# Optimization experiments

Measured on AMD Instinct MI355X. Metric: run time of the kernel, lower is better.

## Reference

```python
import jax, jax.numpy as jnp
import numpy as np

CH = 512
HEADS = 8
REDUCTION = 2
INNER = max(CH // REDUCTION, HEADS)  # 256
POS_RES = 16
LN_EPS = 1e-5


def setup_inputs() -> dict:
    key = jax.random.key(0)
    ks = jax.random.split(key, 7)
    B, H, W = 1, 64, 64
    x = jax.random.normal(ks[0], (B, CH, H, W), dtype=jnp.float32)
    w_qkv = jax.random.normal(ks[1], (INNER * 3, CH), dtype=jnp.float32) * 0.02
    w_proj = jax.random.normal(ks[2], (CH, INNER), dtype=jnp.float32) * 0.02
    b_proj = jnp.zeros((CH,), dtype=jnp.float32)
    pos_bias = jax.random.normal(ks[3], (1, HEADS, POS_RES, POS_RES), dtype=jnp.float32) * 0.02
    gamma = jnp.ones((CH,), dtype=jnp.float32)
    beta = jnp.zeros((CH,), dtype=jnp.float32)
    return {"x": x, "w_qkv": w_qkv, "w_proj": w_proj, "b_proj": b_proj,
            "pos_bias": pos_bias, "gamma": gamma, "beta": beta}


def reference(x, w_qkv, w_proj, b_proj, pos_bias, gamma, beta):
    B, C, H, W = x.shape
    d_head = INNER // HEADS
    scale = jnp.float32(d_head ** -0.5)

    # 1x1 conv == channel matmul
    qkv = jnp.einsum('oc,bchw->bohw', w_qkv, x)  # [B, 3*inner, H, W]
    q, k, v = jnp.split(qkv, 3, axis=1)

    def heads_view(t):
        return t.reshape(B, HEADS, d_head, H * W)  # [B, h, d, HW]

    q, k, v = heads_view(q), heads_view(k), heads_view(v)

    attn = jnp.einsum('bhdi,bhdj->bhij', q * scale, k)  # [B, h, HW, HW]

    # bilinear interp of pos bias 16x16 -> HxW (half-pixel, matches align_corners=False)
    pos = jax.image.resize(pos_bias, (1, HEADS, H, W), method='bilinear')
    pos = pos.reshape(1, HEADS, H * W)
    attn = attn + pos[..., :, None] + pos[..., None, :]

    attn = jax.nn.softmax(attn, axis=-1)
    y = jnp.einsum('bhij,bhdj->bhdi', attn, v)  # [B, h, d, HW]
    y = y.reshape(B, INNER, H, W)

    y = jnp.einsum('co,bohw->bchw', w_proj, y) + b_proj[None, :, None, None]

    # LayerNorm over channel dim of (x + y)
    z = (x + y).transpose(0, 2, 3, 1)  # [B, H, W, C]
    mu = jnp.mean(z, axis=-1, keepdims=True)
    var = jnp.var(z, axis=-1, keepdims=True)
    z = (z - mu) / jnp.sqrt(var + LN_EPS) * gamma + beta
    return z.transpose(0, 3, 1, 2)
```

## Files before the change

### kernel.cpp

```cpp
#include <hip/hip_runtime.h>
#include <hip/hip_bf16.h>
#include <math.h>

#define HW 4096
#define LN_EPS 1e-5f

typedef _Float16 half4v __attribute__((ext_vector_type(4)));
typedef _Float16 half8v __attribute__((ext_vector_type(8)));
typedef float float4v __attribute__((ext_vector_type(4)));

#if __has_builtin(__builtin_amdgcn_exp2f)
#define EXP2F(x) __builtin_amdgcn_exp2f(x)
#else
#define EXP2F(x) exp2f(x)
#endif

__device__ __forceinline__ half4v lo4(half8v v) { return __builtin_shufflevector(v, v, 0, 1, 2, 3); }
__device__ __forceinline__ half4v hi4(half8v v) { return __builtin_shufflevector(v, v, 4, 5, 6, 7); }

__global__ void k_prep(const float* __restrict__ wq, const float* __restrict__ wp,
                       const float* __restrict__ pb,
                       _Float16* __restrict__ wqh, _Float16* __restrict__ wph,
                       float* __restrict__ pos) {
    const float qs = 0.17677669529663687f * 1.4426950408889634f;
    int i = blockIdx.x * 256 + threadIdx.x;
    if (i < 49152) {
        float s = (i < 16384) ? qs : 1.0f;
        float4v a = *(const float4v*)(wq + i * 8);
        float4v b = *(const float4v*)(wq + i * 8 + 4);
        half8v h;
        #pragma unroll
        for (int k = 0; k < 4; k++) { h[k] = (_Float16)(a[k] * s); h[4 + k] = (_Float16)(b[k] * s); }
        *(half8v*)(wqh + i * 8) = h;
    } else if (i < 65536) {
        int j = i - 49152;
        float4v a = *(const float4v*)(wp + j * 8);
        float4v b = *(const float4v*)(wp + j * 8 + 4);
        half8v h;
        #pragma unroll
        for (int k = 0; k < 4; k++) { h[k] = (_Float16)a[k]; h[4 + k] = (_Float16)b[k]; }
        *(half8v*)(wph + j * 8) = h;
    } else {
        int j = i - 65536;
        int h = j >> 12, p = j & 4095, y = p >> 6, x = p & 63;
        float sy = y * 0.25f - 0.375f, sx = x * 0.25f - 0.375f;
        float fy = floorf(sy), fx = floorf(sx);
        float wy = sy - fy, wx = sx - fx;
        int y0 = (int)fy, x0 = (int)fx;
        int y1 = y0 + 1 < 15 ? y0 + 1 : 15;
        int x1 = x0 + 1 < 15 ? x0 + 1 : 15;
        y0 = y0 > 0 ? y0 : 0;
        x0 = x0 > 0 ? x0 : 0;
        const float* src = pb + h * 256;
        float v = (1.f - wy) * ((1.f - wx) * src[y0 * 16 + x0] + wx * src[y0 * 16 + x1]) +
                  wy * ((1.f - wx) * src[y1 * 16 + x0] + wx * src[y1 * 16 + x1]);
        pos[j] = v * 1.4426950408889634f;
    }
}

__global__ __launch_bounds__(256) void k_xt(const float* __restrict__ x,
                                            _Float16* __restrict__ xt) {
    __shared__ _Float16 tile[64][65];
    int c0 = (blockIdx.x >> 6) * 64;
    int p0 = (blockIdx.x & 63) * 64;
    int t = threadIdx.x, w = t >> 6, lane = t & 63;
    #pragma unroll
    for (int r = 0; r < 16; r++)
        tile[w * 16 + r][lane] = (_Float16)x[(c0 + w * 16 + r) * HW + p0 + lane];
    __syncthreads();
    #pragma unroll
    for (int r = 0; r < 16; r++)
        xt[(p0 + w * 16 + r) * 512 + c0 + lane] = tile[lane][w * 16 + r];
}

__global__ __launch_bounds__(256) void k_qkv(const _Float16* __restrict__ wqh,
                                             const _Float16* __restrict__ xt,
                                             _Float16* __restrict__ qa,
                                             _Float16* __restrict__ ka,
                                             _Float16* __restrict__ va) {
    int n0 = (blockIdx.x >> 5) * 64;
    int p0 = (blockIdx.x & 31) * 128;
    int t = threadIdx.x, w = t >> 6, lane = t & 63, quad = lane >> 4, l16 = lane & 15;

    const _Float16* aptr0 = xt + (p0 + w * 16 + l16) * 512 + quad * 8;
    const _Float16* aptr1 = aptr0 + 64 * 512;
    const _Float16* bptr = wqh + (n0 + l16) * 512 + quad * 8;

    float4v acc[2][4] = {};
    #pragma unroll 4
    for (int kc = 0; kc < 16; kc++) {
        half8v a0 = *(const half8v*)(aptr0 + kc * 32);
        half8v a1 = *(const half8v*)(aptr1 + kc * 32);
        #pragma unroll
        for (int nt = 0; nt < 4; nt++) {
            half8v b = *(const half8v*)(bptr + nt * 16 * 512 + kc * 32);
            acc[0][nt] = __builtin_amdgcn_mfma_f32_16x16x32_f16(a0, b, acc[0][nt], 0, 0, 0);
            acc[1][nt] = __builtin_amdgcn_mfma_f32_16x16x32_f16(a1, b, acc[1][nt], 0, 0, 0);
        }
    }
    #pragma unroll
    for (int ps = 0; ps < 2; ps++) {
        #pragma unroll
        for (int nt = 0; nt < 4; nt++) {
            int o = n0 + nt * 16 + l16;
            #pragma unroll
            for (int r = 0; r < 4; r++) {
                int p = p0 + ps * 64 + w * 16 + quad * 4 + r;
                _Float16 v = (_Float16)acc[ps][nt][r];
                if (o < 256) {
                    qa[(o >> 5) * 131072 + p * 32 + (o & 31)] = v;
                } else if (o < 512) {
                    int oc = o - 256, hh = oc >> 5, d = oc & 31;
                    ka[hh * 131072 + (p >> 4) * 512 + ((d >> 3) * 16 + (p & 15)) * 8 + (d & 7)] = v;
                } else {
                    int oc = o - 512, hh = oc >> 5, d = oc & 31;
                    va[hh * 131072 + (p >> 4) * 512 + (((p >> 2) & 3) * 16 + (d & 15)) * 8 +
                       (d >> 4) * 4 + (p & 3)] = v;
                }
            }
        }
    }
}

__global__ __launch_bounds__(256) void k_attn(const _Float16* __restrict__ qa,
                                              const _Float16* __restrict__ ka,
                                              const _Float16* __restrict__ va,
                                              const float* __restrict__ pos,
                                              float* __restrict__ op,
                                              float* __restrict__ lp) {
    __shared__ __attribute__((aligned(16))) _Float16 kbuf[2][2048];
    __shared__ __attribute__((aligned(16))) _Float16 vbuf[2][2048];
    __shared__ __attribute__((aligned(16))) float posl[2048];
    int h = blockIdx.x & 7;
    int jh = (blockIdx.x >> 3) & 1;
    int qb = blockIdx.x >> 4;
    int t = threadIdx.x, w = t >> 6, lane = t & 63, quad = lane >> 4, l16 = lane & 15;
    int q0 = qb * 128 + w * 32;

    float* opp = op + jh * 1048576;
    float* lpp = lp + jh * 32768;

    {
        const float* ps_ = pos + h * HW + jh * 2048;
        *(float4v*)(posl + t * 8) = *(const float4v*)(ps_ + t * 8);
        *(float4v*)(posl + t * 8 + 4) = *(const float4v*)(ps_ + t * 8 + 4);
    }
    half8v qf0 = *(const half8v*)(qa + h * 131072 + (q0 + l16) * 32 + quad * 8);
    half8v qf1 = *(const half8v*)(qa + h * 131072 + (q0 + 16 + l16) * 32 + quad * 8);

    const _Float16* kg = ka + h * 131072 + jh * 65536;
    const _Float16* vg = va + h * 131072 + jh * 65536;

    half8v kreg = *(const half8v*)(kg + t * 8);
    half8v vreg = *(const half8v*)(vg + t * 8);

    float4v o00 = {}, o01 = {}, o10 = {}, o11 = {};
    float lsum0 = 0.f, lsum1 = 0.f;
    const float4v zero = {0.f, 0.f, 0.f, 0.f};

    for (int tile = 0; tile < 32; tile++) {
        int buf = tile & 1;
        *(half8v*)(kbuf[buf] + t * 8) = kreg;
        *(half8v*)(vbuf[buf] + t * 8) = vreg;
        __syncthreads();
        if (tile + 1 < 32) {
            kreg = *(const half8v*)(kg + (tile + 1) * 2048 + t * 8);
            vreg = *(const half8v*)(vg + (tile + 1) * 2048 + t * 8);
        }
        #pragma unroll
        for (int w16 = 0; w16 < 4; w16++) {
            half8v kf = *(const half8v*)(kbuf[buf] + w16 * 512 + lane * 8);
            half8v vf = *(const half8v*)(vbuf[buf] + w16 * 512 + lane * 8);
            float4v pb = *(const float4v*)(posl + tile * 64 + w16 * 16 + quad * 4);

            float4v s0 = __builtin_amdgcn_mfma_f32_16x16x32_f16(kf, qf0, zero, 0, 0, 0);
            float4v s1 = __builtin_amdgcn_mfma_f32_16x16x32_f16(kf, qf1, zero, 0, 0, 0);

            float e0 = EXP2F(s0[0] + pb[0]);
            float e1 = EXP2F(s0[1] + pb[1]);
            float e2 = EXP2F(s0[2] + pb[2]);
            float e3 = EXP2F(s0[3] + pb[3]);
            float f0 = EXP2F(s1[0] + pb[0]);
            float f1 = EXP2F(s1[1] + pb[1]);
            float f2 = EXP2F(s1[2] + pb[2]);
            float f3 = EXP2F(s1[3] + pb[3]);
            lsum0 += (e0 + e1) + (e2 + e3);
            lsum1 += (f0 + f1) + (f2 + f3);

            half4v pa0, pa1;
            pa0[0] = (_Float16)e0; pa0[1] = (_Float16)e1;
            pa0[2] = (_Float16)e2; pa0[3] = (_Float16)e3;
            pa1[0] = (_Float16)f0; pa1[1] = (_Float16)f1;
            pa1[2] = (_Float16)f2; pa1[3] = (_Float16)f3;

            o00 = __builtin_amdgcn_mfma_f32_16x16x16f16(pa0, lo4(vf), o00, 0, 0, 0);
            o01 = __builtin_amdgcn_mfma_f32_16x16x16f16(pa0, hi4(vf), o01, 0, 0, 0);
            o10 = __builtin_amdgcn_mfma_f32_16x16x16f16(pa1, lo4(vf), o10, 0, 0, 0);
            o11 = __builtin_amdgcn_mfma_f32_16x16x16f16(pa1, hi4(vf), o11, 0, 0, 0);
        }
    }
    lsum0 += __shfl_xor(lsum0, 16, 64);
    lsum0 += __shfl_xor(lsum0, 32, 64);
    lsum1 += __shfl_xor(lsum1, 16, 64);
    lsum1 += __shfl_xor(lsum1, 32, 64);
    #pragma unroll
    for (int r = 0; r < 4; r++) {
        int qr = quad * 4 + r;
        int qi0 = q0 + qr, qi1 = q0 + 16 + qr;
        opp[qi0 * 256 + h * 32 + l16] = o00[r];
        opp[qi0 * 256 + h * 32 + 16 + l16] = o01[r];
        opp[qi1 * 256 + h * 32 + l16] = o10[r];
        opp[qi1 * 256 + h * 32 + 16 + l16] = o11[r];
    }
    if (quad == 0) {
        lpp[(q0 + l16) * 8 + h] = lsum0;
        lpp[(q0 + 16 + l16) * 8 + h] = lsum1;
    }
}

__global__ __launch_bounds__(1024) void k_proj_ln(const _Float16* __restrict__ wph,
                                                  const float* __restrict__ op,
                                                  const float* __restrict__ lp,
                                                  const float* __restrict__ x,
                                                  const float* __restrict__ b_proj,
                                                  const float* __restrict__ gamma,
                                                  const float* __restrict__ beta,
                                                  float* __restrict__ out) {
    __shared__ __attribute__((aligned(16))) _Float16 ys[16 * 264];
    __shared__ float red[2][16][17];
    int p0 = blockIdx.x * 16;
    int t = threadIdx.x, w = t >> 6, lane = t & 63, quad = lane >> 4, l16 = lane & 15;
    {
        int p = t >> 6;
        int cg = (t & 63) * 4;
        int pi = p0 + p;
        float4v a = *(const float4v*)(op + pi * 256 + cg);
        float4v b = *(const float4v*)(op + 1048576 + pi * 256 + cg);
        int hh = cg >> 5;
        float l = lp[pi * 8 + hh] + lp[32768 + pi * 8 + hh];
        float inv = 1.f / l;
        half4v y;
        #pragma unroll
        for (int k = 0; k < 4; k++) y[k] = (_Float16)((a[k] + b[k]) * inv);
        *(half4v*)(ys + p * 264 + cg) = y;
    }
    __syncthreads();
    float4v acc[2] = {};
    #pragma unroll
    for (int kc = 0; kc < 8; kc++) {
        half8v b = *(const half8v*)(ys + l16 * 264 + kc * 32 + quad * 8);
        #pragma unroll
        for (int mt = 0; mt < 2; mt++) {
            half8v a = *(const half8v*)(wph + (w * 32 + mt * 16 + l16) * 256 + kc * 32 + quad * 8);
            acc[mt] = __builtin_amdgcn_mfma_f32_16x16x32_f16(a, b, acc[mt], 0, 0, 0);
        }
    }
    int p = p0 + l16;
    float sum = 0.f, sumsq = 0.f;
    #pragma unroll
    for (int mt = 0; mt < 2; mt++)
        #pragma unroll
        for (int r = 0; r < 4; r++) {
            int c = w * 32 + mt * 16 + quad * 4 + r;
            float v = acc[mt][r] + b_proj[c] + x[c * HW + p];
            acc[mt][r] = v;
            sum += v;
            sumsq += v * v;
        }
    sum += __shfl_xor(sum, 16, 64);
    sum += __shfl_xor(sum, 32, 64);
    sumsq += __shfl_xor(sumsq, 16, 64);
    sumsq += __shfl_xor(sumsq, 32, 64);
    if (quad == 0) { red[0][w][l16] = sum; red[1][w][l16] = sumsq; }
    __syncthreads();
    float s0 = 0.f, s1 = 0.f;
    #pragma unroll
    for (int ww = 0; ww < 16; ww++) { s0 += red[0][ww][l16]; s1 += red[1][ww][l16]; }
    float mean = s0 * (1.f / 512.f);
    float var = s1 * (1.f / 512.f) - mean * mean;
    float rstd = rsqrtf(var + LN_EPS);
    #pragma unroll
    for (int mt = 0; mt < 2; mt++)
        #pragma unroll
        for (int r = 0; r < 4; r++) {
            int c = w * 32 + mt * 16 + quad * 4 + r;
            out[c * HW + p] = (acc[mt][r] - mean) * rstd * gamma[c] + beta[c];
        }
}

extern "C" void kernel_launch(void* const* d_in, const int* in_sizes, int n_in,
                              void* d_out, int out_size, void* d_ws, size_t ws_size,
                              hipStream_t stream) {
    const float* x      = (const float*)d_in[0];
    const float* w_qkv  = (const float*)d_in[1];
    const float* w_proj = (const float*)d_in[2];
    const float* b_proj = (const float*)d_in[3];
    const float* pos_b  = (const float*)d_in[4];
    const float* gamma  = (const float*)d_in[5];
    const float* beta   = (const float*)d_in[6];
    char* ws = (char*)d_ws;
    _Float16* xt  = (_Float16*)(ws);
    _Float16* qa  = (_Float16*)(ws + 4194304);
    _Float16* ka  = (_Float16*)(ws + 6291456);
    _Float16* va  = (_Float16*)(ws + 8388608);
    float*    op  = (float*)   (ws + 10485760);
    float*    lp  = (float*)   (ws + 18874368);
    float*    pos = (float*)   (ws + 19136512);
    _Float16* wqh = (_Float16*)(ws + 19267584);
    _Float16* wph = (_Float16*)(ws + 20054016);

    k_prep<<<384, 256, 0, stream>>>(w_qkv, w_proj, pos_b, wqh, wph, pos);
    k_xt<<<512, 256, 0, stream>>>(x, xt);
    k_qkv<<<384, 256, 0, stream>>>(wqh, xt, qa, ka, va);
    k_attn<<<512, 256, 0, stream>>>(qa, ka, va, pos, op, lp);
    k_proj_ln<<<256, 1024, 0, stream>>>(wph, op, lp, x, b_proj, gamma, beta, (float*)d_out);
}
```

Measured before the change: 151.0 us.

## Split attention keys four ways, fuse prep kernels, use direct LDS loads

Merges the transpose and weight-prep kernels into one launch and vectorizes the transpose stores. Attention now splits the key range into four chunks instead of two, doubling the grid to 1024 blocks with a 4-blocks-per-CU launch bound. It streams K/V tiles straight into LDS with global_load_lds, folds the position bias into the MFMA accumulator input, and uses packed conversions plus fdot2 for the row sums. The projection kernel then reduces four partial outputs, which costs more workspace and more partial-sum traffic.

```diff
diff --git a/kernel.cpp b/kernel.cpp
--- a/kernel.cpp
+++ b/kernel.cpp
@@ -8,6 +8,8 @@
 typedef _Float16 half4v __attribute__((ext_vector_type(4)));
 typedef _Float16 half8v __attribute__((ext_vector_type(8)));
 typedef float float4v __attribute__((ext_vector_type(4)));
+typedef __fp16 fp16v2 __attribute__((ext_vector_type(2)));
+typedef __fp16 fp16v4 __attribute__((ext_vector_type(4)));
 
 #if __has_builtin(__builtin_amdgcn_exp2f)
 #define EXP2F(x) __builtin_amdgcn_exp2f(x)
@@ -18,12 +20,47 @@
 __device__ __forceinline__ half4v lo4(half8v v) { return __builtin_shufflevector(v, v, 0, 1, 2, 3); }
 __device__ __forceinline__ half4v hi4(half8v v) { return __builtin_shufflevector(v, v, 4, 5, 6, 7); }
 
-__global__ void k_prep(const float* __restrict__ wq, const float* __restrict__ wp,
-                       const float* __restrict__ pb,
-                       _Float16* __restrict__ wqh, _Float16* __restrict__ wph,
-                       float* __restrict__ pos) {
+__device__ __forceinline__ void gload_lds16(const _Float16* g, _Float16* l) {
+#if __has_builtin(__builtin_amdgcn_global_load_lds)
+    __builtin_amdgcn_global_load_lds(
+        (const __attribute__((address_space(1))) void*)(const void*)g,
+        (__attribute__((address_space(3))) void*)(void*)l, 16, 0, 0);
+#else
+    int lane = threadIdx.x & 63;
+    *(half8v*)(l + lane * 8) = *(const half8v*)g;
+#endif
+}
+
+__global__ __launch_bounds__(256) void k_pre(const float* __restrict__ x,
+                                             const float* __restrict__ wq,
+                                             const float* __restrict__ wp,
+                                             const float* __restrict__ pb,
+                                             _Float16* __restrict__ xt,
+                                             _Float16* __restrict__ wqh,
+                                             _Float16* __restrict__ wph,
+                                             float* __restrict__ pos) {
+    int bx = blockIdx.x, t = threadIdx.x;
+    if (bx < 512) {
+        __shared__ _Float16 tile[64][65];
+        int c0 = (bx >> 6) * 64, p0 = (bx & 63) * 64;
+        int w = t >> 6, lane = t & 63;
+        #pragma unroll
+        for (int r = 0; r < 16; r++)
+            tile[w * 16 + r][lane] = (_Float16)x[(c0 + w * 16 + r) * HW + p0 + lane];
+        __syncthreads();
+        int cg = (t & 15) * 4, pr = t >> 4;
+        #pragma unroll
+        for (int r = 0; r < 4; r++) {
+            int p = pr + r * 16;
+            half4v v;
+            #pragma unroll
+            for (int k = 0; k < 4; k++) v[k] = tile[cg + k][p];
+            *(half4v*)&xt[(p0 + p) * 512 + c0 + cg] = v;
+        }
+        return;
+    }
+    int i = (bx - 512) * 256 + t;
     const float qs = 0.17677669529663687f * 1.4426950408889634f;
-    int i = blockIdx.x * 256 + threadIdx.x;
     if (i < 49152) {
         float s = (i < 16384) ? qs : 1.0f;
         float4v a = *(const float4v*)(wq + i * 8);
@@ -42,8 +79,8 @@
         *(half8v*)(wph + j * 8) = h;
     } else {
         int j = i - 65536;
-        int h = j >> 12, p = j & 4095, y = p >> 6, x = p & 63;
-        float sy = y * 0.25f - 0.375f, sx = x * 0.25f - 0.375f;
+        int h = j >> 12, p = j & 4095, y = p >> 6, xx = p & 63;
+        float sy = y * 0.25f - 0.375f, sx = xx * 0.25f - 0.375f;
         float fy = floorf(sy), fx = floorf(sx);
         float wy = sy - fy, wx = sx - fx;
         int y0 = (int)fy, x0 = (int)fx;
@@ -56,21 +93,6 @@
                   wy * ((1.f - wx) * src[y1 * 16 + x0] + wx * src[y1 * 16 + x1]);
         pos[j] = v * 1.4426950408889634f;
     }
-}
-
-__global__ __launch_bounds__(256) void k_xt(const float* __restrict__ x,
-                                            _Float16* __restrict__ xt) {
-    __shared__ _Float16 tile[64][65];
-    int c0 = (blockIdx.x >> 6) * 64;
-    int p0 = (blockIdx.x & 63) * 64;
-    int t = threadIdx.x, w = t >> 6, lane = t & 63;
-    #pragma unroll
-    for (int r = 0; r < 16; r++)
-        tile[w * 16 + r][lane] = (_Float16)x[(c0 + w * 16 + r) * HW + p0 + lane];
-    __syncthreads();
-    #pragma unroll
-    for (int r = 0; r < 16; r++)
-        xt[(p0 + w * 16 + r) * 512 + c0 + lane] = tile[lane][w * 16 + r];
 }
 
 __global__ __launch_bounds__(256) void k_qkv(const _Float16* __restrict__ wqh,
@@ -122,77 +144,80 @@
     }
 }
 
-__global__ __launch_bounds__(256) void k_attn(const _Float16* __restrict__ qa,
-                                              const _Float16* __restrict__ ka,
-                                              const _Float16* __restrict__ va,
-                                              const float* __restrict__ pos,
-                                              float* __restrict__ op,
-                                              float* __restrict__ lp) {
+__global__ __launch_bounds__(256, 4) void k_attn(const _Float16* __restrict__ qa,
+                                                 const _Float16* __restrict__ ka,
+                                                 const _Float16* __restrict__ va,
+                                                 const float* __restrict__ pos,
+                                                 float* __restrict__ op,
+                                                 float* __restrict__ lp) {
     __shared__ __attribute__((aligned(16))) _Float16 kbuf[2][2048];
     __shared__ __attribute__((aligned(16))) _Float16 vbuf[2][2048];
-    __shared__ __attribute__((aligned(16))) float posl[2048];
+    __shared__ __attribute__((aligned(16))) float posl[1024];
     int h = blockIdx.x & 7;
-    int jh = (blockIdx.x >> 3) & 1;
-    int qb = blockIdx.x >> 4;
+    int jq = (blockIdx.x >> 3) & 3;
+    int qb = blockIdx.x >> 5;
     int t = threadIdx.x, w = t >> 6, lane = t & 63, quad = lane >> 4, l16 = lane & 15;
     int q0 = qb * 128 + w * 32;
 
-    float* opp = op + jh * 1048576;
-    float* lpp = lp + jh * 32768;
-
-    {
-        const float* ps_ = pos + h * HW + jh * 2048;
-        *(float4v*)(posl + t * 8) = *(const float4v*)(ps_ + t * 8);
-        *(float4v*)(posl + t * 8 + 4) = *(const float4v*)(ps_ + t * 8 + 4);
-    }
+    float* opp = op + jq * 1048576;
+    float* lpp = lp + jq * 32768;
+
+    *(float4v*)(posl + t * 4) = *(const float4v*)(pos + h * HW + jq * 1024 + t * 4);
+
     half8v qf0 = *(const half8v*)(qa + h * 131072 + (q0 + l16) * 32 + quad * 8);
     half8v qf1 = *(const half8v*)(qa + h * 131072 + (q0 + 16 + l16) * 32 + quad * 8);
 
-    const _Float16* kg = ka + h * 131072 + jh * 65536;
-    const _Float16* vg = va + h * 131072 + jh * 65536;
-
-    half8v kreg = *(const half8v*)(kg + t * 8);
-    half8v vreg = *(const half8v*)(vg + t * 8);
+    const _Float16* kg = ka + h * 131072 + jq * 32768;
+    const _Float16* vg = va + h * 131072 + jq * 32768;
+
+    gload_lds16(kg + (w * 64 + lane) * 8, &kbuf[0][w * 512]);
+    gload_lds16(vg + (w * 64 + lane) * 8, &vbuf[0][w * 512]);
 
     float4v o00 = {}, o01 = {}, o10 = {}, o11 = {};
     float lsum0 = 0.f, lsum1 = 0.f;
-    const float4v zero = {0.f, 0.f, 0.f, 0.f};
-
-    for (int tile = 0; tile < 32; tile++) {
+    const fp16v2 one2 = {(__fp16)1.0f, (__fp16)1.0f};
+
+    for (int tile = 0; tile < 16; tile++) {
         int buf = tile & 1;
-        *(half8v*)(kbuf[buf] + t * 8) = kreg;
-        *(half8v*)(vbuf[buf] + t * 8) = vreg;
         __syncthreads();
-        if (tile + 1 < 32) {
-            kreg = *(const half8v*)(kg + (tile + 1) * 2048 + t * 8);
-            vreg = *(const half8v*)(vg + (tile + 1) * 2048 + t * 8);
+        if (tile + 1 < 16) {
+            gload_lds16(kg + (tile + 1) * 2048 + (w * 64 + lane) * 8, &kbuf[buf ^ 1][w * 512]);
+            gload_lds16(vg + (tile + 1) * 2048 + (w * 64 + lane) * 8, &vbuf[buf ^ 1][w * 512]);
         }
         #pragma unroll
         for (int w16 = 0; w16 < 4; w16++) {
             half8v kf = *(const half8v*)(kbuf[buf] + w16 * 512 + lane * 8);
             half8v vf = *(const half8v*)(vbuf[buf] + w16 * 512 + lane * 8);
-            float4v pb = *(const float4v*)(posl + tile * 64 + w16 * 16 + quad * 4);
-
-            float4v s0 = __builtin_amdgcn_mfma_f32_16x16x32_f16(kf, qf0, zero, 0, 0, 0);
-            float4v s1 = __builtin_amdgcn_mfma_f32_16x16x32_f16(kf, qf1, zero, 0, 0, 0);
-
-            float e0 = EXP2F(s0[0] + pb[0]);
-            float e1 = EXP2F(s0[1] + pb[1]);
-            float e2 = EXP2F(s0[2] + pb[2]);
-            float e3 = EXP2F(s0[3] + pb[3]);
-            float f0 = EXP2F(s1[0] + pb[0]);
-            float f1 = EXP2F(s1[1] + pb[1]);
-            float f2 = EXP2F(s1[2] + pb[2]);
-            float f3 = EXP2F(s1[3] + pb[3]);
+            float4v pbv = *(const float4v*)(posl + tile * 64 + w16 * 16 + quad * 4);
+
+            float4v s0 = __builtin_amdgcn_mfma_f32_16x16x32_f16(kf, qf0, pbv, 0, 0, 0);
+            float4v s1 = __builtin_amdgcn_mfma_f32_16x16x32_f16(kf, qf1, pbv, 0, 0, 0);
+
+            float e0 = EXP2F(s0[0]);
+            float e1 = EXP2F(s0[1]);
+            float e2 = EXP2F(s0[2]);
+            float e3 = EXP2F(s0[3]);
+            float f0 = EXP2F(s1[0]);
+            float f1 = EXP2F(s1[1]);
+            float f2 = EXP2F(s1[2]);
+            float f3 = EXP2F(s1[3]);
+
+            fp16v2 a01 = __builtin_amdgcn_cvt_pkrtz(e0, e1);
+            fp16v2 a23 = __builtin_amdgcn_cvt_pkrtz(e2, e3);
+            fp16v2 b01 = __builtin_amdgcn_cvt_pkrtz(f0, f1);
+            fp16v2 b23 = __builtin_amdgcn_cvt_pkrtz(f2, f3);
+            half4v pa0 = __builtin_bit_cast(half4v, __builtin_shufflevector(a01, a23, 0, 1, 2, 3));
+            half4v pa1 = __builtin_bit_cast(half4v, __builtin_shufflevector(b01, b23, 0, 1, 2, 3));
+
+#if __has_builtin(__builtin_amdgcn_fdot2)
+            lsum0 = __builtin_amdgcn_fdot2(a01, one2, lsum0, false);
+            lsum0 = __builtin_amdgcn_fdot2(a23, one2, lsum0, false);
+            lsum1 = __builtin_amdgcn_fdot2(b01, one2, lsum1, false);
+            lsum1 = __builtin_amdgcn_fdot2(b23, one2, lsum1, false);
+#else
             lsum0 += (e0 + e1) + (e2 + e3);
             lsum1 += (f0 + f1) + (f2 + f3);
-
-            half4v pa0, pa1;
-            pa0[0] = (_Float16)e0; pa0[1] = (_Float16)e1;
-            pa0[2] = (_Float16)e2; pa0[3] = (_Float16)e3;
-            pa1[0] = (_Float16)f0; pa1[1] = (_Float16)f1;
-            pa1[2] = (_Float16)f2; pa1[3] = (_Float16)f3;
-
+#endif
             o00 = __builtin_amdgcn_mfma_f32_16x16x16f16(pa0, lo4(vf), o00, 0, 0, 0);
             o01 = __builtin_amdgcn_mfma_f32_16x16x16f16(pa0, hi4(vf), o01, 0, 0, 0);
             o10 = __builtin_amdgcn_mfma_f32_16x16x16f16(pa1, lo4(vf), o10, 0, 0, 0);
@@ -231,17 +256,19 @@
     int p0 = blockIdx.x * 16;
     int t = threadIdx.x, w = t >> 6, lane = t & 63, quad = lane >> 4, l16 = lane & 15;
     {
-        int p = t >> 6;
-        int cg = (t & 63) * 4;
+        int p = t >> 6, cg = (t & 63) * 4;
         int pi = p0 + p;
-        float4v a = *(const float4v*)(op + pi * 256 + cg);
-        float4v b = *(const float4v*)(op + 1048576 + pi * 256 + cg);
+        float4v a0 = *(const float4v*)(op + pi * 256 + cg);
+        float4v a1 = *(const float4v*)(op + 1048576 + pi * 256 + cg);
+        float4v a2 = *(const float4v*)(op + 2097152 + pi * 256 + cg);
+        float4v a3 = *(const float4v*)(op + 3145728 + pi * 256 + cg);
         int hh = cg >> 5;
-        float l = lp[pi * 8 + hh] + lp[32768 + pi * 8 + hh];
+        float l = lp[pi * 8 + hh] + lp[32768 + pi * 8 + hh] +
+                  lp[65536 + pi * 8 + hh] + lp[98304 + pi * 8 + hh];
         float inv = 1.f / l;
         half4v y;
         #pragma unroll
-        for (int k = 0; k < 4; k++) y[k] = (_Float16)((a[k] + b[k]) * inv);
+        for (int k = 0; k < 4; k++) y[k] = (_Float16)(((a0[k] + a1[k]) + (a2[k] + a3[k])) * inv);
         *(half4v*)(ys + p * 264 + cg) = y;
     }
     __syncthreads();
@@ -304,14 +331,13 @@
     _Float16* ka  = (_Float16*)(ws + 6291456);
     _Float16* va  = (_Float16*)(ws + 8388608);
     float*    op  = (float*)   (ws + 10485760);
-    float*    lp  = (float*)   (ws + 18874368);
-    float*    pos = (float*)   (ws + 19136512);
-    _Float16* wqh = (_Float16*)(ws + 19267584);
-    _Float16* wph = (_Float16*)(ws + 20054016);
-
-    k_prep<<<384, 256, 0, stream>>>(w_qkv, w_proj, pos_b, wqh, wph, pos);
-    k_xt<<<512, 256, 0, stream>>>(x, xt);
+    float*    lp  = (float*)   (ws + 27262976);
+    float*    pos = (float*)   (ws + 27787264);
+    _Float16* wqh = (_Float16*)(ws + 27918336);
+    _Float16* wph = (_Float16*)(ws + 28704768);
+
+    k_pre<<<896, 256, 0, stream>>>(x, w_qkv, w_proj, pos_b, xt, wqh, wph, pos);
     k_qkv<<<384, 256, 0, stream>>>(wqh, xt, qa, ka, va);
-    k_attn<<<512, 256, 0, stream>>>(qa, ka, va, pos, op, lp);
+    k_attn<<<1024, 256, 0, stream>>>(qa, ka, va, pos, op, lp);
     k_proj_ln<<<256, 1024, 0, stream>>>(wph, op, lp, x, b_proj, gamma, beta, (float*)d_out);
 }
```

After: 139.9 us. 7.4% less time.
